# Kernel tuning notes

Measured on AMD Instinct MI355X. Metric: run time of the kernel, lower is better.

Reference implementation:

```python
import jax, jax.numpy as jnp
import numpy as np

# Static config (Swin-T stage 1, SW-MSA)
B = 32; H = 56; W = 56; C = 96; NH = 3; WS = 7; SHIFT = 3
N = WS * WS                 # tokens per window (49)
NW = (H // WS) * (W // WS)  # windows per image (64)
HD = C // NH                # head dim (32)
SCALE = HD ** -0.5
EPS = 1e-3  # keras LayerNormalization default epsilon


def _rel_index():
    # Matches tf.stack(tf.meshgrid(h, w)) with default 'xy' indexing
    xx, yy = np.meshgrid(np.arange(WS), np.arange(WS))
    coords = np.stack([xx, yy]).reshape(2, -1)              # [2, 49]
    rel = (coords[:, :, None] - coords[:, None, :]).transpose(1, 2, 0)
    rel[:, :, 0] += WS - 1
    rel[:, :, 1] += WS - 1
    rel[:, :, 0] *= 2 * WS - 1
    return rel.sum(-1)                                       # [49, 49]

REL_IDX = jnp.asarray(_rel_index())


def _attn_mask():
    # Standard Swin shifted-window attention mask
    img = np.zeros((H, W))
    cnt = 0
    sl = (slice(0, -WS), slice(-WS, -SHIFT), slice(-SHIFT, None))
    for hs in sl:
        for ws_ in sl:
            img[hs, ws_] = cnt
            cnt += 1
    win = img.reshape(H // WS, WS, W // WS, WS).transpose(0, 2, 1, 3).reshape(-1, N)
    diff = win[:, None, :] - win[:, :, None]
    return jnp.asarray(np.where(diff != 0, -100.0, 0.0), dtype=np.float32)  # [nW,49,49]

MASK = _attn_mask()


def _ln(x, g, b):
    mu = x.mean(-1, keepdims=True)
    var = ((x - mu) ** 2).mean(-1, keepdims=True)
    return (x - mu) / jnp.sqrt(var + EPS) * g + b


def setup_inputs() -> dict:
    key = jax.random.key(0)
    ks = jax.random.split(key, 6)
    f32 = jnp.float32
    return {
        "x": jax.random.normal(ks[0], (B, H * W, C), f32),
        "norm1_g": jnp.ones((C,), f32), "norm1_b": jnp.zeros((C,), f32),
        "qkv_w": jax.random.normal(ks[1], (C, 3 * C), f32) * 0.02,
        "qkv_b": jnp.zeros((3 * C,), f32),
        "bias_table": jax.random.normal(ks[2], ((2 * WS - 1) ** 2, NH), f32) * 0.02,
        "proj_w": jax.random.normal(ks[3], (C, C), f32) * 0.02,
        "proj_b": jnp.zeros((C,), f32),
        "norm2_g": jnp.ones((C,), f32), "norm2_b": jnp.zeros((C,), f32),
        "fc1_w": jax.random.normal(ks[4], (C, 4 * C), f32) * 0.02,
        "fc1_b": jnp.zeros((4 * C,), f32),
        "fc2_w": jax.random.normal(ks[5], (4 * C, C), f32) * 0.02,
        "fc2_b": jnp.zeros((C,), f32),
    }


def reference(x, norm1_g, norm1_b, qkv_w, qkv_b, bias_table, proj_w, proj_b,
              norm2_g, norm2_b, fc1_w, fc1_b, fc2_w, fc2_b):
    shortcut = x
    h = _ln(x, norm1_g, norm1_b).reshape(B, H, W, C)
    # cyclic shift (SW-MSA)
    h = jnp.roll(h, (-SHIFT, -SHIFT), axis=(1, 2))
    # window partition -> [B*nW, N, C]
    h = h.reshape(B, H // WS, WS, W // WS, WS, C).transpose(0, 1, 3, 2, 4, 5).reshape(-1, N, C)
    qkv = (h @ qkv_w + qkv_b).reshape(-1, N, 3, NH, HD).transpose(2, 0, 3, 1, 4)
    q, k, v = qkv[0], qkv[1], qkv[2]            # each [B*nW, NH, N, HD]
    attn = jnp.einsum('bhnd,bhmd->bhnm', q * SCALE, k)
    bias = bias_table[REL_IDX.reshape(-1)].reshape(N, N, NH).transpose(2, 0, 1)
    attn = attn + bias[None]
    attn = attn.reshape(B, NW, NH, N, N) + MASK[None, :, None]
    attn = attn.reshape(-1, NH, N, N)
    # NOTE: source applies softmax twice (once in branch, once unconditionally)
    attn = jax.nn.softmax(jax.nn.softmax(attn, axis=-1), axis=-1)
    o = jnp.einsum('bhnm,bhmd->bhnd', attn, v).transpose(0, 2, 1, 3).reshape(-1, N, C)
    o = o @ proj_w + proj_b
    # window reverse + reverse cyclic shift
    o = o.reshape(B, H // WS, W // WS, WS, WS, C).transpose(0, 1, 3, 2, 4, 5).reshape(B, H, W, C)
    o = jnp.roll(o, (SHIFT, SHIFT), axis=(1, 2)).reshape(B, H * W, C)
    x = shortcut + o
    y = _ln(x, norm2_g, norm2_b)
    # NOTE: source Mlp applies gelu in Dense activation AND again in call -> double gelu
    y = jax.nn.gelu(y @ fc1_w + fc1_b, approximate=False)
    y = jax.nn.gelu(y, approximate=False)
    y = y @ fc2_w + fc2_b
    return x + y
```

## Files before the change

kernel.cpp:

```cpp
#include <hip/hip_runtime.h>
#include <math.h>

#define BB   32
#define HH   56
#define WWI  56
#define CC   96
#define NHD  3
#define WSZ  7
#define SHF  3
#define NTK  49
#define NWIN 64
#define HDM  32
#define TOT  (BB*HH*WWI)
#define QKSCALE 0.17677669529663687f
#define LEPS 1e-3f

typedef __attribute__((ext_vector_type(8))) short s8v;
typedef __attribute__((ext_vector_type(4))) float fx4;
typedef unsigned long long ull_t;

#define MFMA16(a,b,c) __builtin_amdgcn_mfma_f32_16x16x32_bf16((a),(b),(c),0,0,0)

__device__ __forceinline__ unsigned short f2bf(float f) {
    union { float f; unsigned u; } v; v.f = f;
    unsigned r = v.u + 0x7FFFu + ((v.u >> 16) & 1u);
    return (unsigned short)(r >> 16);
}

__device__ __forceinline__ float gelu_t(float x) {
    float x3 = x * x * x;
    float z = -1.5957691216f * fmaf(0.044715f, x3, x);
    return x * __builtin_amdgcn_rcpf(1.f + __expf(z));
}

__device__ __forceinline__ int wtok_to_orig(int wt) {
    int win = wt / NTK;
    int p   = wt - win * NTK;
    int b   = win >> 6;
    int w   = win & 63;
    int wi = w >> 3, wj = w & 7;
    int pi = p / WSZ, pj = p - pi * WSZ;
    int r = wi * WSZ + pi + SHF; if (r >= HH) r -= HH;
    int c = wj * WSZ + pj + SHF; if (c >= WWI) c -= WWI;
    return b * (HH * WWI) + r * WWI + c;
}

__device__ __forceinline__ void ln_frag(const float* __restrict__ row,
                                        const float* __restrict__ gg,
                                        const float* __restrict__ bb,
                                        int g4, s8v ha[3])
{
    float h[24];
    #pragma unroll
    for (int ks = 0; ks < 3; ++ks) {
        fx4 v0 = *reinterpret_cast<const fx4*>(row + ks * 32 + g4 * 8);
        fx4 v1 = *reinterpret_cast<const fx4*>(row + ks * 32 + g4 * 8 + 4);
        h[ks*8+0]=v0.x; h[ks*8+1]=v0.y; h[ks*8+2]=v0.z; h[ks*8+3]=v0.w;
        h[ks*8+4]=v1.x; h[ks*8+5]=v1.y; h[ks*8+6]=v1.z; h[ks*8+7]=v1.w;
    }
    float s = 0.f, s2 = 0.f;
    #pragma unroll
    for (int j = 0; j < 24; ++j) { s += h[j]; s2 = fmaf(h[j], h[j], s2); }
    s  += __shfl_xor(s, 16);  s  += __shfl_xor(s, 32);
    s2 += __shfl_xor(s2, 16); s2 += __shfl_xor(s2, 32);
    const float mu = s * (1.f/CC);
    const float rs = rsqrtf(s2 * (1.f/CC) - mu * mu + LEPS);
    #pragma unroll
    for (int ks = 0; ks < 3; ++ks) {
        union { s8v v; unsigned short u[8]; } p;
        #pragma unroll
        for (int j = 0; j < 8; ++j) {
            int c = ks * 32 + g4 * 8 + j;
            p.u[j] = f2bf((h[ks*8+j] - mu) * rs * gg[c] + bb[c]);
        }
        ha[ks] = p.v;
    }
}

extern "C" __global__ void p0_prep(const float* __restrict__ qw, const float* __restrict__ pw,
                                   const float* __restrict__ w1, const float* __restrict__ w2,
                                   const float* __restrict__ btab,
                                   unsigned short* __restrict__ wsw)
{
    int i = blockIdx.x * 256 + threadIdx.x;
    if (i < 27648) {
        int n = i / 96, k = i - n * 96;
        float v = qw[k * 288 + n];
        if (n < 96) v *= QKSCALE;
        wsw[i] = f2bf(v);
    } else if (i < 36864) {
        int j = i - 27648; int n = j / 96, k = j - n * 96;
        wsw[i] = f2bf(pw[k * 96 + n]);
    } else if (i < 73728) {
        int j = i - 36864;
        int e = j & 7, f = j >> 3;
        int lane = f & 63, fid = f >> 6;
        int ks = fid % 3, t = fid / 3;
        int nt = t & 3, ck = t >> 2;
        int n = ck * 64 + nt * 16 + (lane & 15);
        int k = ks * 32 + (lane >> 4) * 8 + e;
        wsw[i] = f2bf(w1[k * 384 + n]);
    } else if (i < 110592) {
        int j = i - 73728;
        int e = j & 7, f = j >> 3;
        int lane = f & 63, fid = f >> 6;
        int ks = fid & 1, t = fid >> 1;
        int nt = t % 6, ck = t / 6;
        int n = nt * 16 + (lane & 15);
        int k = ck * 64 + ks * 32 + (lane >> 4) * 8 + e;
        wsw[i] = f2bf(w2[k * 96 + n]);
    } else if (i < 148224) {
        float* bm = (float*)(wsw + 110592);
        int j = i - 110592;
        int n = j & 63, mh = j >> 6;
        int m = mh % 49, t = mh / 49;
        int hd = t % 3, cls = t / 3;
        float val = 0.f;
        if (n < 49) {
            int it = m / 7, jt = m - it * 7;
            int iu = n / 7, ju = n - iu * 7;
            int li  = (cls & 2) ? (it < 4 ? 1 : 2) : 0;
            int lj  = (cls & 1) ? (jt < 4 ? 1 : 2) : 0;
            int lui = (cls & 2) ? (iu < 4 ? 1 : 2) : 0;
            int luj = (cls & 1) ? (ju < 4 ? 1 : 2) : 0;
            int bidx = (jt - ju + 6) * 13 + (it - iu + 6);
            val = btab[bidx * 3 + hd] + ((li*3+lj) == (lui*3+luj) ? 0.f : -100.f);
        }
        bm[j] = val;
    }
}

#define LDH 104
extern "C" __global__ void __launch_bounds__(512, 4) k1_qkv(
    const float* __restrict__ x, const float* __restrict__ g1, const float* __restrict__ b1,
    const unsigned short* __restrict__ qwt, const float* __restrict__ qb,
    unsigned short* __restrict__ qkvb)
{
    __shared__ unsigned short Wc[96 * LDH];
    const int tid = threadIdx.x, wave = tid >> 6, lane = tid & 63;
    const int l15 = lane & 15, g4 = lane >> 4;
    const int blk = blockIdx.x;

    s8v ha[3];
    {
        const int orig = wtok_to_orig(blk * 128 + wave * 16 + l15);
        ln_frag(x + (size_t)orig * CC, g1, b1, g4, ha);
    }

    for (int ck = 0; ck < 3; ++ck) {
        for (int i = tid; i < 96 * 12; i += 512) {
            int r = i / 12, k0 = (i - r * 12) * 8;
            *reinterpret_cast<s8v*>(&Wc[r * LDH + k0]) =
                *reinterpret_cast<const s8v*>(&qwt[(ck * 96 + r) * 96 + k0]);
        }
        __syncthreads();
        fx4 acc[6];
        #pragma unroll
        for (int nt = 0; nt < 6; ++nt) acc[nt] = (fx4){0.f,0.f,0.f,0.f};
        #pragma unroll
        for (int ks = 0; ks < 3; ++ks) {
            #pragma unroll
            for (int nt = 0; nt < 6; ++nt) {
                s8v b = *reinterpret_cast<const s8v*>(&Wc[(nt*16 + l15)*LDH + ks*32 + g4*8]);
                acc[nt] = MFMA16(ha[ks], b, acc[nt]);
            }
        }
        const int rowb = blk * 128 + wave * 16 + g4 * 4;
        const float qmul = (ck == 0) ? QKSCALE : 1.f;
        #pragma unroll
        for (int nt = 0; nt < 6; ++nt) {
            const int col = ck * 96 + nt * 16 + l15;
            const float qbc = qb[col] * qmul;
            #pragma unroll
            for (int r = 0; r < 4; ++r)
                qkvb[(size_t)(rowb + r) * 288 + col] = f2bf(acc[nt][r] + qbc);
        }
        __syncthreads();
    }
}

extern "C" __global__ void __launch_bounds__(64, 2) k2_attn(
    unsigned short* __restrict__ qkvb, const float* __restrict__ bm)
{
    __shared__ unsigned short P[64][72];
    const int lane = threadIdx.x;
    const int l15 = lane & 15, g4 = lane >> 4;
    const int task = blockIdx.x;
    const int win = task / 3, h = task - win * 3;
    const int g0  = win * NTK;
    const int w   = win & 63;
    const int cls = (((w >> 3) == 7) ? 2 : 0) + (((w & 7) == 7) ? 1 : 0);
    const float* BMh = bm + ((size_t)(cls * 3 + h)) * 49 * 64;

    s8v aq[4], bk[4];
    #pragma unroll
    for (int mt = 0; mt < 4; ++mt) {
        int tok = mt * 16 + l15; if (tok > 48) tok = 48;
        const unsigned short* qp = &qkvb[(size_t)(g0 + tok) * 288 + h * HDM + g4 * 8];
        aq[mt] = *reinterpret_cast<const s8v*>(qp);
        bk[mt] = *reinterpret_cast<const s8v*>(qp + 96);
    }

    fx4 sc[4][4];
    #pragma unroll
    for (int mt = 0; mt < 4; ++mt)
        #pragma unroll
        for (int nt = 0; nt < 4; ++nt)
            sc[mt][nt] = MFMA16(aq[mt], bk[nt], ((fx4){0.f,0.f,0.f,0.f}));

    #pragma unroll
    for (int mt = 0; mt < 4; ++mt) {
        #pragma unroll
        for (int r = 0; r < 4; ++r) {
            const int m = mt * 16 + g4 * 4 + r;
            const int mc = m > 48 ? 48 : m;
            float rs1 = 0.f;
            #pragma unroll
            for (int nt = 0; nt < 4; ++nt) {
                const int n = nt * 16 + l15;
                float s = sc[mt][nt][r] + BMh[mc * 64 + n];
                float e = (n < NTK) ? __expf(s) : 0.f;
                sc[mt][nt][r] = e;
                rs1 += e;
            }
            rs1 += __shfl_xor(rs1, 1); rs1 += __shfl_xor(rs1, 2);
            rs1 += __shfl_xor(rs1, 4); rs1 += __shfl_xor(rs1, 8);
            const float iv1 = 1.f / rs1;
            float rs2 = 0.f;
            #pragma unroll
            for (int nt = 0; nt < 4; ++nt) {
                const int n = nt * 16 + l15;
                float e2 = (n < NTK) ? __expf(sc[mt][nt][r] * iv1) : 0.f;
                sc[mt][nt][r] = e2;
                rs2 += e2;
            }
            rs2 += __shfl_xor(rs2, 1); rs2 += __shfl_xor(rs2, 2);
            rs2 += __shfl_xor(rs2, 4); rs2 += __shfl_xor(rs2, 8);
            const float iv2 = 1.f / rs2;
            #pragma unroll
            for (int nt = 0; nt < 4; ++nt)
                P[m][nt * 16 + l15] = f2bf(sc[mt][nt][r] * iv2);
        }
    }
    __syncthreads();

    fx4 oc[4][2];
    #pragma unroll
    for (int mt = 0; mt < 4; ++mt) { oc[mt][0] = (fx4){0.f,0.f,0.f,0.f}; oc[mt][1] = (fx4){0.f,0.f,0.f,0.f}; }
    #pragma unroll
    for (int ks = 0; ks < 2; ++ks) {
        s8v vb[2];
        #pragma unroll
        for (int nt = 0; nt < 2; ++nt) {
            union { s8v v; unsigned short u[8]; } pv;
            #pragma unroll
            for (int j = 0; j < 8; ++j) {
                int tok = ks * 32 + g4 * 8 + j; if (tok > 48) tok = 48;
                pv.u[j] = qkvb[(size_t)(g0 + tok) * 288 + 192 + h * HDM + nt * 16 + l15];
            }
            vb[nt] = pv.v;
        }
        #pragma unroll
        for (int mt = 0; mt < 4; ++mt) {
            s8v pa = *reinterpret_cast<const s8v*>(&P[mt * 16 + l15][ks * 32 + g4 * 8]);
            oc[mt][0] = MFMA16(pa, vb[0], oc[mt][0]);
            oc[mt][1] = MFMA16(pa, vb[1], oc[mt][1]);
        }
    }
    #pragma unroll
    for (int mt = 0; mt < 4; ++mt) {
        #pragma unroll
        for (int r = 0; r < 4; ++r) {
            const int m = mt * 16 + g4 * 4 + r;
            if (m < NTK) {
                qkvb[(size_t)(g0 + m) * 288 + h * HDM + l15]      = f2bf(oc[mt][0][r]);
                qkvb[(size_t)(g0 + m) * 288 + h * HDM + 16 + l15] = f2bf(oc[mt][1][r]);
            }
        }
    }
}

extern "C" __global__ void __launch_bounds__(512, 4) k2b_proj(
    const unsigned short* __restrict__ qkvb, const unsigned short* __restrict__ pwt,
    const float* __restrict__ pb, const float* __restrict__ x, float* __restrict__ out)
{
    __shared__ unsigned short Wc[96 * LDH];
    const int tid = threadIdx.x, wave = tid >> 6, lane = tid & 63;
    const int l15 = lane & 15, g4 = lane >> 4;
    const int blk = blockIdx.x;

    for (int i = tid; i < 96 * 12; i += 512) {
        int r = i / 12, k0 = (i - r * 12) * 8;
        *reinterpret_cast<s8v*>(&Wc[r * LDH + k0]) =
            *reinterpret_cast<const s8v*>(&pwt[r * 96 + k0]);
    }
    const unsigned short* arow = qkvb + (size_t)(blk * 128 + wave * 16 + l15) * 288 + g4 * 8;
    s8v a0 = *reinterpret_cast<const s8v*>(arow);
    s8v a1 = *reinterpret_cast<const s8v*>(arow + 32);
    s8v a2 = *reinterpret_cast<const s8v*>(arow + 64);
    __syncthreads();

    fx4 acc[6];
    #pragma unroll
    for (int nt = 0; nt < 6; ++nt) acc[nt] = (fx4){0.f,0.f,0.f,0.f};
    #pragma unroll
    for (int nt = 0; nt < 6; ++nt) {
        acc[nt] = MFMA16(a0, *reinterpret_cast<const s8v*>(&Wc[(nt*16 + l15)*LDH +  0 + g4*8]), acc[nt]);
        acc[nt] = MFMA16(a1, *reinterpret_cast<const s8v*>(&Wc[(nt*16 + l15)*LDH + 32 + g4*8]), acc[nt]);
        acc[nt] = MFMA16(a2, *reinterpret_cast<const s8v*>(&Wc[(nt*16 + l15)*LDH + 64 + g4*8]), acc[nt]);
    }
    int orig[4];
    #pragma unroll
    for (int r = 0; r < 4; ++r)
        orig[r] = wtok_to_orig(blk * 128 + wave * 16 + g4 * 4 + r);
    #pragma unroll
    for (int nt = 0; nt < 6; ++nt) {
        const int col = nt * 16 + l15;
        const float pbc = pb[col];
        #pragma unroll
        for (int r = 0; r < 4; ++r) {
            const size_t idx = (size_t)orig[r] * CC + col;
            out[idx] = acc[nt][r] + pbc + x[idx];
        }
    }
}

#define LDA 72
extern "C" __global__ void __launch_bounds__(256, 3) k3_mlp(
    float* __restrict__ xio, const float* __restrict__ g2, const float* __restrict__ b2,
    const unsigned short* __restrict__ w1f, const float* __restrict__ bf1,
    const unsigned short* __restrict__ w2f, const float* __restrict__ bf2)
{
    __shared__ unsigned short Ac[64 * LDA];
    const int tid = threadIdx.x, wave = tid >> 6, lane = tid & 63;
    const int l15 = lane & 15, g4 = lane >> 4;
    const int row0 = blockIdx.x * 64 + wave * 16;

    s8v ha[3];
    ln_frag(xio + (size_t)(row0 + l15) * CC, g2, b2, g4, ha);

    fx4 oacc[6];
    #pragma unroll
    for (int nt = 0; nt < 6; ++nt) oacc[nt] = (fx4){0.f,0.f,0.f,0.f};

    for (int ck = 0; ck < 6; ++ck) {
        fx4 a1[4];
        #pragma unroll
        for (int nt = 0; nt < 4; ++nt) a1[nt] = (fx4){0.f,0.f,0.f,0.f};
        #pragma unroll
        for (int ks = 0; ks < 3; ++ks) {
            #pragma unroll
            for (int nt = 0; nt < 4; ++nt) {
                s8v b = *reinterpret_cast<const s8v*>(
                    &w1f[(((ck * 4 + nt) * 3 + ks) * 64 + lane) * 8]);
                a1[nt] = MFMA16(ha[ks], b, a1[nt]);
            }
        }
        #pragma unroll
        for (int nt = 0; nt < 4; ++nt) {
            const float bb = bf1[ck * 64 + nt * 16 + l15];
            #pragma unroll
            for (int r = 0; r < 4; ++r) {
                float v0 = a1[nt][r] + bb;
                Ac[(wave*16 + g4*4 + r) * LDA + nt*16 + l15] = f2bf(gelu_t(gelu_t(v0)));
            }
        }
        #pragma unroll
        for (int ks = 0; ks < 2; ++ks) {
            s8v a = *reinterpret_cast<const s8v*>(&Ac[(wave*16 + l15)*LDA + ks*32 + g4*8]);
            #pragma unroll
            for (int nt = 0; nt < 6; ++nt) {
                s8v b = *reinterpret_cast<const s8v*>(
                    &w2f[(((ck * 6 + nt) * 2 + ks) * 64 + lane) * 8]);
                oacc[nt] = MFMA16(a, b, oacc[nt]);
            }
        }
    }

    const int rowb = row0 + g4 * 4;
    #pragma unroll
    for (int nt = 0; nt < 6; ++nt) {
        const int col = nt * 16 + l15;
        const float bb = bf2[col];
        #pragma unroll
        for (int r = 0; r < 4; ++r) {
            const size_t idx = (size_t)(rowb + r) * CC + col;
            xio[idx] = xio[idx] + oacc[nt][r] + bb;
        }
    }
}

extern "C" void kernel_launch(void* const* d_in, const int* in_sizes, int n_in,
                              void* d_out, int out_size, void* d_ws, size_t ws_size,
                              hipStream_t stream)
{
    const float* x    = (const float*)d_in[0];
    const float* n1g  = (const float*)d_in[1];
    const float* n1b  = (const float*)d_in[2];
    const float* qw   = (const float*)d_in[3];
    const float* qb   = (const float*)d_in[4];
    const float* btab = (const float*)d_in[5];
    const float* pw   = (const float*)d_in[6];
    const float* pb   = (const float*)d_in[7];
    const float* n2g  = (const float*)d_in[8];
    const float* n2b  = (const float*)d_in[9];
    const float* w1   = (const float*)d_in[10];
    const float* bf1  = (const float*)d_in[11];
    const float* w2   = (const float*)d_in[12];
    const float* bf2  = (const float*)d_in[13];
    float* out = (float*)d_out;

    unsigned short* qkvb = (unsigned short*)d_ws;
    unsigned short* wbf = qkvb + (size_t)TOT * 288;
    unsigned short* qwt = wbf;
    unsigned short* pwt = qwt + 27648;
    unsigned short* w1f = pwt + 9216;
    unsigned short* w2f = w1f + 36864;
    float* bmt = (float*)(wbf + 110592);

    p0_prep <<<579, 256, 0, stream>>>(qw, pw, w1, w2, btab, wbf);
    k1_qkv  <<<TOT/128, 512, 0, stream>>>(x, n1g, n1b, qwt, qb, qkvb);
    k2_attn <<<BB*NWIN*NHD, 64, 0, stream>>>(qkvb, bmt);
    k2b_proj<<<TOT/128, 512, 0, stream>>>(qkvb, pwt, pb, x, out);
    k3_mlp  <<<TOT/64, 256, 0, stream>>>(out, n2g, n2b, w1f, bf1, w2f, bf2);
}
```

Measured before the change: 141.3 us.

## Prepack qkv/proj weights into MFMA fragment layout and double rows per MLP wave

The prep kernel now stores the QKV and projection weights pre-swizzled into per-lane MFMA fragment order. k1_qkv and k2b_proj read B operands straight from global memory instead of staging them through shared memory, which removes the LDS copies and barriers and lets them run as smaller 256-thread blocks. k3_mlp processes 32 rows per wave so each weight fragment load feeds two MFMAs, halving weight traffic per row. The cost is more global/L2 weight reads in k1 and k2b, plus higher register pressure in the MLP kernel.

```diff
diff --git a/kernel.cpp b/kernel.cpp
--- a/kernel.cpp
+++ b/kernel.cpp
@@ -84,12 +84,22 @@
 {
     int i = blockIdx.x * 256 + threadIdx.x;
     if (i < 27648) {
-        int n = i / 96, k = i - n * 96;
+        int e = i & 7, f = i >> 3;
+        int lane = f & 63, fid = f >> 6;
+        int ks = fid % 3, t = fid / 3;
+        int nt = t % 6, ck = t / 6;
+        int n = ck * 96 + nt * 16 + (lane & 15);
+        int k = ks * 32 + (lane >> 4) * 8 + e;
         float v = qw[k * 288 + n];
         if (n < 96) v *= QKSCALE;
         wsw[i] = f2bf(v);
     } else if (i < 36864) {
-        int j = i - 27648; int n = j / 96, k = j - n * 96;
+        int j = i - 27648;
+        int e = j & 7, f = j >> 3;
+        int lane = f & 63, fid = f >> 6;
+        int ks = fid % 3, nt = fid / 3;
+        int n = nt * 16 + (lane & 15);
+        int k = ks * 32 + (lane >> 4) * 8 + e;
         wsw[i] = f2bf(pw[k * 96 + n]);
     } else if (i < 73728) {
         int j = i - 36864;
@@ -130,30 +140,23 @@
     }
 }
 
-#define LDH 104
-extern "C" __global__ void __launch_bounds__(512, 4) k1_qkv(
+extern "C" __global__ void __launch_bounds__(256, 3) k1_qkv(
     const float* __restrict__ x, const float* __restrict__ g1, const float* __restrict__ b1,
-    const unsigned short* __restrict__ qwt, const float* __restrict__ qb,
+    const unsigned short* __restrict__ qwtf, const float* __restrict__ qb,
     unsigned short* __restrict__ qkvb)
 {
-    __shared__ unsigned short Wc[96 * LDH];
     const int tid = threadIdx.x, wave = tid >> 6, lane = tid & 63;
     const int l15 = lane & 15, g4 = lane >> 4;
-    const int blk = blockIdx.x;
+    const int row0 = blockIdx.x * 64 + wave * 16;
 
     s8v ha[3];
     {
-        const int orig = wtok_to_orig(blk * 128 + wave * 16 + l15);
+        const int orig = wtok_to_orig(row0 + l15);
         ln_frag(x + (size_t)orig * CC, g1, b1, g4, ha);
     }
 
+    #pragma unroll 1
     for (int ck = 0; ck < 3; ++ck) {
-        for (int i = tid; i < 96 * 12; i += 512) {
-            int r = i / 12, k0 = (i - r * 12) * 8;
-            *reinterpret_cast<s8v*>(&Wc[r * LDH + k0]) =
-                *reinterpret_cast<const s8v*>(&qwt[(ck * 96 + r) * 96 + k0]);
-        }
-        __syncthreads();
         fx4 acc[6];
         #pragma unroll
         for (int nt = 0; nt < 6; ++nt) acc[nt] = (fx4){0.f,0.f,0.f,0.f};
@@ -161,11 +164,12 @@
         for (int ks = 0; ks < 3; ++ks) {
             #pragma unroll
             for (int nt = 0; nt < 6; ++nt) {
-                s8v b = *reinterpret_cast<const s8v*>(&Wc[(nt*16 + l15)*LDH + ks*32 + g4*8]);
+                s8v b = *reinterpret_cast<const s8v*>(
+                    &qwtf[(((ck * 6 + nt) * 3 + ks) * 64 + lane) * 8]);
                 acc[nt] = MFMA16(ha[ks], b, acc[nt]);
             }
         }
-        const int rowb = blk * 128 + wave * 16 + g4 * 4;
+        const int rowb = row0 + g4 * 4;
         const float qmul = (ck == 0) ? QKSCALE : 1.f;
         #pragma unroll
         for (int nt = 0; nt < 6; ++nt) {
@@ -175,7 +179,6 @@
             for (int r = 0; r < 4; ++r)
                 qkvb[(size_t)(rowb + r) * 288 + col] = f2bf(acc[nt][r] + qbc);
         }
-        __syncthreads();
     }
 }
 
@@ -280,39 +283,35 @@
     }
 }
 
-extern "C" __global__ void __launch_bounds__(512, 4) k2b_proj(
-    const unsigned short* __restrict__ qkvb, const unsigned short* __restrict__ pwt,
+extern "C" __global__ void __launch_bounds__(256, 3) k2b_proj(
+    const unsigned short* __restrict__ qkvb, const unsigned short* __restrict__ pwtf,
     const float* __restrict__ pb, const float* __restrict__ x, float* __restrict__ out)
 {
-    __shared__ unsigned short Wc[96 * LDH];
     const int tid = threadIdx.x, wave = tid >> 6, lane = tid & 63;
     const int l15 = lane & 15, g4 = lane >> 4;
-    const int blk = blockIdx.x;
-
-    for (int i = tid; i < 96 * 12; i += 512) {
-        int r = i / 12, k0 = (i - r * 12) * 8;
-        *reinterpret_cast<s8v*>(&Wc[r * LDH + k0]) =
-            *reinterpret_cast<const s8v*>(&pwt[r * 96 + k0]);
-    }
-    const unsigned short* arow = qkvb + (size_t)(blk * 128 + wave * 16 + l15) * 288 + g4 * 8;
-    s8v a0 = *reinterpret_cast<const s8v*>(arow);
-    s8v a1 = *reinterpret_cast<const s8v*>(arow + 32);
-    s8v a2 = *reinterpret_cast<const s8v*>(arow + 64);
-    __syncthreads();
+    const int row0 = blockIdx.x * 64 + wave * 16;
+
+    const unsigned short* arow = qkvb + (size_t)(row0 + l15) * 288 + g4 * 8;
+    s8v a[3];
+    a[0] = *reinterpret_cast<const s8v*>(arow);
+    a[1] = *reinterpret_cast<const s8v*>(arow + 32);
+    a[2] = *reinterpret_cast<const s8v*>(arow + 64);
 
     fx4 acc[6];
     #pragma unroll
     for (int nt = 0; nt < 6; ++nt) acc[nt] = (fx4){0.f,0.f,0.f,0.f};
     #pragma unroll
-    for (int nt = 0; nt < 6; ++nt) {
-        acc[nt] = MFMA16(a0, *reinterpret_cast<const s8v*>(&Wc[(nt*16 + l15)*LDH +  0 + g4*8]), acc[nt]);
-        acc[nt] = MFMA16(a1, *reinterpret_cast<const s8v*>(&Wc[(nt*16 + l15)*LDH + 32 + g4*8]), acc[nt]);
-        acc[nt] = MFMA16(a2, *reinterpret_cast<const s8v*>(&Wc[(nt*16 + l15)*LDH + 64 + g4*8]), acc[nt]);
+    for (int ks = 0; ks < 3; ++ks) {
+        #pragma unroll
+        for (int nt = 0; nt < 6; ++nt) {
+            s8v b = *reinterpret_cast<const s8v*>(&pwtf[((nt * 3 + ks) * 64 + lane) * 8]);
+            acc[nt] = MFMA16(a[ks], b, acc[nt]);
+        }
     }
     int orig[4];
     #pragma unroll
     for (int r = 0; r < 4; ++r)
-        orig[r] = wtok_to_orig(blk * 128 + wave * 16 + g4 * 4 + r);
+        orig[r] = wtok_to_orig(row0 + g4 * 4 + r);
     #pragma unroll
     for (int nt = 0; nt < 6; ++nt) {
         const int col = nt * 16 + l15;
@@ -331,61 +330,65 @@
     const unsigned short* __restrict__ w1f, const float* __restrict__ bf1,
     const unsigned short* __restrict__ w2f, const float* __restrict__ bf2)
 {
-    __shared__ unsigned short Ac[64 * LDA];
+    __shared__ unsigned short Ac[128 * LDA];
     const int tid = threadIdx.x, wave = tid >> 6, lane = tid & 63;
     const int l15 = lane & 15, g4 = lane >> 4;
-    const int row0 = blockIdx.x * 64 + wave * 16;
-
-    s8v ha[3];
-    ln_frag(xio + (size_t)(row0 + l15) * CC, g2, b2, g4, ha);
-
-    fx4 oacc[6];
-    #pragma unroll
-    for (int nt = 0; nt < 6; ++nt) oacc[nt] = (fx4){0.f,0.f,0.f,0.f};
-
+    const int row0 = blockIdx.x * 128 + wave * 32;
+
+    s8v ha0[3], ha1[3];
+    ln_frag(xio + (size_t)(row0 + l15) * CC,      g2, b2, g4, ha0);
+    ln_frag(xio + (size_t)(row0 + 16 + l15) * CC, g2, b2, g4, ha1);
+
+    fx4 oa0[6], oa1[6];
+    #pragma unroll
+    for (int nt = 0; nt < 6; ++nt) { oa0[nt] = (fx4){0.f,0.f,0.f,0.f}; oa1[nt] = (fx4){0.f,0.f,0.f,0.f}; }
+
+    #pragma unroll 1
     for (int ck = 0; ck < 6; ++ck) {
-        fx4 a1[4];
-        #pragma unroll
-        for (int nt = 0; nt < 4; ++nt) a1[nt] = (fx4){0.f,0.f,0.f,0.f};
-        #pragma unroll
-        for (int ks = 0; ks < 3; ++ks) {
-            #pragma unroll
-            for (int nt = 0; nt < 4; ++nt) {
+        #pragma unroll
+        for (int nt = 0; nt < 4; ++nt) {
+            fx4 aA = (fx4){0.f,0.f,0.f,0.f}, aB = (fx4){0.f,0.f,0.f,0.f};
+            #pragma unroll
+            for (int ks = 0; ks < 3; ++ks) {
                 s8v b = *reinterpret_cast<const s8v*>(
                     &w1f[(((ck * 4 + nt) * 3 + ks) * 64 + lane) * 8]);
-                a1[nt] = MFMA16(ha[ks], b, a1[nt]);
-            }
-        }
-        #pragma unroll
-        for (int nt = 0; nt < 4; ++nt) {
+                aA = MFMA16(ha0[ks], b, aA);
+                aB = MFMA16(ha1[ks], b, aB);
+            }
             const float bb = bf1[ck * 64 + nt * 16 + l15];
             #pragma unroll
             for (int r = 0; r < 4; ++r) {
-                float v0 = a1[nt][r] + bb;
-                Ac[(wave*16 + g4*4 + r) * LDA + nt*16 + l15] = f2bf(gelu_t(gelu_t(v0)));
+                Ac[(wave*32 +      g4*4 + r) * LDA + nt*16 + l15] = f2bf(gelu_t(gelu_t(aA[r] + bb)));
+                Ac[(wave*32 + 16 + g4*4 + r) * LDA + nt*16 + l15] = f2bf(gelu_t(gelu_t(aB[r] + bb)));
             }
         }
         #pragma unroll
         for (int ks = 0; ks < 2; ++ks) {
-            s8v a = *reinterpret_cast<const s8v*>(&Ac[(wave*16 + l15)*LDA + ks*32 + g4*8]);
+            s8v pA = *reinterpret_cast<const s8v*>(&Ac[(wave*32 +      l15)*LDA + ks*32 + g4*8]);
+            s8v pB = *reinterpret_cast<const s8v*>(&Ac[(wave*32 + 16 + l15)*LDA + ks*32 + g4*8]);
             #pragma unroll
             for (int nt = 0; nt < 6; ++nt) {
                 s8v b = *reinterpret_cast<const s8v*>(
                     &w2f[(((ck * 6 + nt) * 2 + ks) * 64 + lane) * 8]);
-                oacc[nt] = MFMA16(a, b, oacc[nt]);
-            }
-        }
-    }
-
-    const int rowb = row0 + g4 * 4;
-    #pragma unroll
-    for (int nt = 0; nt < 6; ++nt) {
-        const int col = nt * 16 + l15;
-        const float bb = bf2[col];
-        #pragma unroll
-        for (int r = 0; r < 4; ++r) {
-            const size_t idx = (size_t)(rowb + r) * CC + col;
-            xio[idx] = xio[idx] + oacc[nt][r] + bb;
+                oa0[nt] = MFMA16(pA, b, oa0[nt]);
+                oa1[nt] = MFMA16(pB, b, oa1[nt]);
+            }
+        }
+    }
+
+    #pragma unroll
+    for (int u = 0; u < 2; ++u) {
+        const int rowb = row0 + u * 16 + g4 * 4;
+        #pragma unroll
+        for (int nt = 0; nt < 6; ++nt) {
+            const int col = nt * 16 + l15;
+            const float bb = bf2[col];
+            #pragma unroll
+            for (int r = 0; r < 4; ++r) {
+                const size_t idx = (size_t)(rowb + r) * CC + col;
+                const float ov = (u == 0) ? oa0[nt][r] : oa1[nt][r];
+                xio[idx] = xio[idx] + ov + bb;
+            }
         }
     }
 }
@@ -411,16 +414,16 @@
     float* out = (float*)d_out;
 
     unsigned short* qkvb = (unsigned short*)d_ws;
-    unsigned short* wbf = qkvb + (size_t)TOT * 288;
-    unsigned short* qwt = wbf;
-    unsigned short* pwt = qwt + 27648;
-    unsigned short* w1f = pwt + 9216;
-    unsigned short* w2f = w1f + 36864;
+    unsigned short* wbf  = qkvb + (size_t)TOT * 288;
+    unsigned short* qwtf = wbf;
+    unsigned short* pwtf = qwtf + 27648;
+    unsigned short* w1f  = pwtf + 9216;
+    unsigned short* w2f  = w1f + 36864;
     float* bmt = (float*)(wbf + 110592);
 
     p0_prep <<<579, 256, 0, stream>>>(qw, pw, w1, w2, btab, wbf);
-    k1_qkv  <<<TOT/128, 512, 0, stream>>>(x, n1g, n1b, qwt, qb, qkvb);
+    k1_qkv  <<<TOT/64, 256, 0, stream>>>(x, n1g, n1b, qwtf, qb, qkvb);
     k2_attn <<<BB*NWIN*NHD, 64, 0, stream>>>(qkvb, bmt);
-    k2b_proj<<<TOT/128, 512, 0, stream>>>(qkvb, pwt, pb, x, out);
-    k3_mlp  <<<TOT/64, 256, 0, stream>>>(out, n2g, n2b, w1f, bf1, w2f, bf2);
-}
+    k2b_proj<<<TOT/64, 256, 0, stream>>>(qkvb, pwtf, pb, x, out);
+    k3_mlp  <<<TOT/128, 256, 0, stream>>>(out, n2g, n2b, w1f, bf1, w2f, bf2);
+}
```

Result: slower. 157.2 us (+11.2%).
